# Kernel optimization log

Measured on AMD Instinct MI355X. Metric: run time of the kernel, lower is better.

The kernel has to match this reference:

```python
import jax, jax.numpy as jnp
import numpy as np
import math

B, N = 1, 512
C_S, C_Z, C_H, H = 384, 128, 16, 12
P_Q, P_V, NBINS = 4, 8, 64
OUT_DIM = H * (C_H + P_V * 4 + C_Z)


def setup_inputs() -> dict:
    key = jax.random.key(0)
    ks = jax.random.split(key, 16)
    def rn(k, shape, scale=1.0):
        return jax.random.normal(k, shape, dtype=jnp.float32) * scale
    rotations, _ = jnp.linalg.qr(rn(ks[3], (B, N, 3, 3)))  # orthogonal frames
    w = 0.02
    return {
        "s": rn(ks[0], (B, N, C_S)),
        "z": rn(ks[1], (B, N, N, C_Z)),
        "translations": rn(ks[2], (B, N, 3), 10.0),  # spread over ~0-32 A bins
        "rotations": rotations,
        "Wq": rn(ks[4], (C_S, H * C_H), w), "bq": jnp.zeros((H * C_H,), jnp.float32),
        "Wk": rn(ks[5], (C_S, H * C_H), w), "bk": jnp.zeros((H * C_H,), jnp.float32),
        "Wv": rn(ks[6], (C_S, H * C_H), w), "bv": jnp.zeros((H * C_H,), jnp.float32),
        "Wqp": rn(ks[7], (C_S, H * P_Q * 3), w), "bqp": jnp.zeros((H * P_Q * 3,), jnp.float32),
        "Wkp": rn(ks[8], (C_S, H * P_Q * 3), w), "bkp": jnp.zeros((H * P_Q * 3,), jnp.float32),
        "Wvp": rn(ks[9], (C_S, H * P_V * 3), w), "bvp": jnp.zeros((H * P_V * 3,), jnp.float32),
        "Wb": rn(ks[10], (C_Z, H), w), "bb": jnp.zeros((H,), jnp.float32),
        "emb": rn(ks[11], (NBINS, H), w),
        "scale_logits": jnp.zeros((3, H), jnp.float32),
        "head_weights": jnp.ones((H,), jnp.float32),
        "Wout": rn(ks[12], (OUT_DIM, C_S), w), "bout": jnp.zeros((C_S,), jnp.float32),
    }


def reference(s, z, translations, rotations, Wq, bq, Wk, bk, Wv, bv, Wqp, bqp, Wkp, bkp, Wvp, bvp, Wb, bb, emb, scale_logits, head_weights, Wout, bout):
    b, n, _ = s.shape
    t = translations
    q = (s @ Wq + bq).reshape(b, n, H, C_H)
    k = (s @ Wk + bk).reshape(b, n, H, C_H)
    v = (s @ Wv + bv).reshape(b, n, H, C_H)
    q_pts = (s @ Wqp + bqp).reshape(b, n, H, P_Q, 3)
    k_pts = (s @ Wkp + bkp).reshape(b, n, H, P_Q, 3)
    v_pts = (s @ Wvp + bvp).reshape(b, n, H, P_V, 3)
    # local -> global frame
    q_g = jnp.einsum('bnij,bnhpj->bnhpi', rotations, q_pts) + t[:, :, None, None, :]
    k_g = jnp.einsum('bnij,bnhpj->bnhpi', rotations, k_pts) + t[:, :, None, None, :]
    v_g = jnp.einsum('bnij,bnhpj->bnhpi', rotations, v_pts) + t[:, :, None, None, :]
    scalar_logits = jnp.einsum('bnhc,bmhc->bnmh', q, k) / math.sqrt(C_H)  # [b,n,m,h]
    point_dist = jnp.sum((q_g[:, :, None] - k_g[:, None]) ** 2, axis=-1)  # [b,n,m,h,p]
    point_logits = -0.5 * jnp.sum(point_dist, axis=-1) * head_weights[None, None, None, :]
    pair_bias = z @ Wb + bb  # [b,n,m,h]
    pair_dist = jnp.linalg.norm(t[:, :, None, :] - t[:, None, :, :], axis=-1)  # [b,n,m]
    edges = jnp.linspace(0.0, 32.0, NBINS + 1)
    bins = jnp.clip(jnp.searchsorted(edges, pair_dist, side='left') - 1, 0, NBINS - 1)
    dist_bias = emb[bins]  # [b,n,m,h]
    scales = jnp.stack([
        (pair_dist <= 5.0).astype(s.dtype),
        ((pair_dist > 5.0) & (pair_dist <= 15.0)).astype(s.dtype),
        jnp.ones_like(pair_dist),
    ], axis=-1)  # [b,n,m,3]
    per_head = jax.nn.softmax(scale_logits, axis=0)  # [3,h]
    multiscale = jnp.einsum('bnms,sh->bnmh', scales, per_head)
    logits = scalar_logits + point_logits + pair_bias + dist_bias + multiscale
    attn = jax.nn.softmax(logits.astype(jnp.float32), axis=2).astype(s.dtype)  # over m
    out_scalar = jnp.einsum('bnmh,bmhc->bnhc', attn, v)
    out_pts_g = jnp.einsum('bnmh,bmhpi->bnhpi', attn, v_g)
    # global -> local frame (R^T applied)
    out_pts_l = jnp.einsum('bnji,bnhpj->bnhpi', rotations, out_pts_g - t[:, :, None, None, :])
    out_norms = jnp.linalg.norm(out_pts_l, axis=-1)  # [b,n,h,p]
    pair_feat = jnp.einsum('bnmh,bnmc->bnhc', attn, z)
    feats = jnp.concatenate([
        out_scalar,
        out_pts_l.reshape(b, n, H, P_V * 3),
        out_norms,
        pair_feat,
    ], axis=-1).reshape(b, n, -1)  # [b,n,OUT_DIM]
    return feats @ Wout + bout
```

## Files before the change

### kernel.cpp

```cpp
#include <hip/hip_runtime.h>

#define NTOK 512
#define CS 384
#define CZ 128
#define CH 16
#define HN 12
#define PQ 4
#define PV 8
#define FEAT_DIM 2112
#define HSEG 176

__global__ __launch_bounds__(256) void k_proj(
    const float* __restrict__ s,
    const float* __restrict__ Wq,  const float* __restrict__ bq,
    const float* __restrict__ Wk,  const float* __restrict__ bk,
    const float* __restrict__ Wv,  const float* __restrict__ bv,
    const float* __restrict__ Wqp, const float* __restrict__ bqp,
    const float* __restrict__ Wkp, const float* __restrict__ bkp,
    const float* __restrict__ Wvp, const float* __restrict__ bvp,
    float* __restrict__ qs, float* __restrict__ ksT, float* __restrict__ vs,
    float* __restrict__ raw_g)
{
    __shared__ float s_l[16 * CS];
    __shared__ float Ws[16][64];
    const int t  = threadIdx.x;
    const int n0 = blockIdx.x * 16;

    const float4* sg  = (const float4*)(s + (size_t)n0 * CS);
    float4*       sl4 = (float4*)s_l;
#pragma unroll
    for (int j = 0; j < 6; ++j) sl4[j * 256 + t] = sg[j * 256 + t];

    const int col = blockIdx.y * 64 + (t & 63);
    const int tq  = t >> 6;
    const float* bv_;
    int lc;
    if (col < 192)      { bv_ = bq;  lc = col;       }
    else if (col < 384) { bv_ = bk;  lc = col - 192; }
    else if (col < 576) { bv_ = bv;  lc = col - 384; }
    else if (col < 720) { bv_ = bqp; lc = col - 576; }
    else if (col < 864) { bv_ = bkp; lc = col - 720; }
    else                { bv_ = bvp; lc = col - 864; }

    const int kk_s = t >> 4, cq = t & 15;
    const int gcol = blockIdx.y * 64 + cq * 4;
    const float* Wsrc; int lcs, ncs;
    if (gcol < 192)      { Wsrc = Wq;  lcs = gcol;       ncs = 192; }
    else if (gcol < 384) { Wsrc = Wk;  lcs = gcol - 192; ncs = 192; }
    else if (gcol < 576) { Wsrc = Wv;  lcs = gcol - 384; ncs = 192; }
    else if (gcol < 720) { Wsrc = Wqp; lcs = gcol - 576; ncs = 144; }
    else if (gcol < 864) { Wsrc = Wkp; lcs = gcol - 720; ncs = 144; }
    else                 { Wsrc = Wvp; lcs = gcol - 864; ncs = 288; }

    float a0, a1, a2, a3;
    a0 = a1 = a2 = a3 = bv_[lc];
    __syncthreads();

    for (int ks = 0; ks < CS; ks += 16) {
        float4 w4 = *(const float4*)&Wsrc[(size_t)(ks + kk_s) * ncs + lcs];
        __syncthreads();
        *(float4*)&Ws[kk_s][cq * 4] = w4;
        __syncthreads();
        const float* srow = s_l + tq * 4 * CS + ks;
#pragma unroll
        for (int k4 = 0; k4 < 4; ++k4) {
            float4 s0 = *(const float4*)&srow[k4 * 4];
            float4 s1 = *(const float4*)&srow[CS + k4 * 4];
            float4 s2 = *(const float4*)&srow[2 * CS + k4 * 4];
            float4 s3 = *(const float4*)&srow[3 * CS + k4 * 4];
            float w0 = Ws[k4 * 4 + 0][t & 63];
            float w1 = Ws[k4 * 4 + 1][t & 63];
            float w2 = Ws[k4 * 4 + 2][t & 63];
            float w3 = Ws[k4 * 4 + 3][t & 63];
            a0 += s0.x * w0 + s0.y * w1 + s0.z * w2 + s0.w * w3;
            a1 += s1.x * w0 + s1.y * w1 + s1.z * w2 + s1.w * w3;
            a2 += s2.x * w0 + s2.y * w1 + s2.z * w2 + s2.w * w3;
            a3 += s3.x * w0 + s3.y * w1 + s3.z * w2 + s3.w * w3;
        }
    }

    const int n = n0 + tq * 4;
    if (col < 192) {
        qs[(size_t)(n + 0) * 192 + lc] = a0;
        qs[(size_t)(n + 1) * 192 + lc] = a1;
        qs[(size_t)(n + 2) * 192 + lc] = a2;
        qs[(size_t)(n + 3) * 192 + lc] = a3;
    } else if (col < 384) {
        float* p = ksT + (size_t)lc * NTOK + n;
        p[0] = a0; p[1] = a1; p[2] = a2; p[3] = a3;
    } else if (col < 576) {
        vs[(size_t)(n + 0) * 192 + lc] = a0;
        vs[(size_t)(n + 1) * 192 + lc] = a1;
        vs[(size_t)(n + 2) * 192 + lc] = a2;
        vs[(size_t)(n + 3) * 192 + lc] = a3;
    } else {
        const int pc = col - 576;
        raw_g[(size_t)(n + 0) * 576 + pc] = a0;
        raw_g[(size_t)(n + 1) * 576 + pc] = a1;
        raw_g[(size_t)(n + 2) * 576 + pc] = a2;
        raw_g[(size_t)(n + 3) * 576 + pc] = a3;
    }
}

__global__ __launch_bounds__(256) void k_frame(
    const float* __restrict__ raw_g,
    const float* __restrict__ trans,
    const float* __restrict__ rot,
    float* __restrict__ qg, float* __restrict__ kgT, float* __restrict__ vg,
    float* __restrict__ transT)
{
    const int e = blockIdx.x * 256 + threadIdx.x;
    if (e < 512 * 576) {
        const int n = e / 576, loc = e % 576;
        const int i = loc % 3, base = loc - i;
        const float* rp = raw_g + (size_t)n * 576 + base;
        float x0 = rp[0], x1 = rp[1], x2 = rp[2];
        const float* R = rot + (size_t)n * 9 + i * 3;
        float v = trans[(size_t)n * 3 + i] + R[0] * x0 + R[1] * x1 + R[2] * x2;
        if (loc < 144)      qg[(size_t)n * 144 + loc] = v;
        else if (loc < 288) kgT[(size_t)(loc - 144) * NTOK + n] = v;
        else                vg[(size_t)n * 288 + loc - 288] = v;
    } else {
        const int idx = e - 512 * 576;
        if (idx < 3 * NTOK) {
            const int m = idx / 3, i = idx % 3;
            transT[(size_t)i * NTOK + m] = trans[(size_t)m * 3 + i];
        }
    }
}

__global__ __launch_bounds__(256, 2) void k_mid(
    const float* __restrict__ z,
    const float* __restrict__ qs, const float* __restrict__ ksT,
    const float* __restrict__ qg, const float* __restrict__ kgT,
    const float* __restrict__ trans, const float* __restrict__ transT,
    const float* __restrict__ Wb, const float* __restrict__ bbv,
    const float* __restrict__ emb, const float* __restrict__ slog,
    const float* __restrict__ hw,
    float* __restrict__ attn, float* __restrict__ feats)
{
    __shared__ __align__(16) float lgT[NTOK * HN];
    __shared__ __align__(16) float zl[64 * 132];
    __shared__ __align__(16) float wbT[HN * CZ];
    __shared__ float embl[64 * HN];
    __shared__ float ql[192];
    __shared__ float qgl[144];
    __shared__ float tl[3];
    __shared__ float phl[36];
    __shared__ float hwl[HN];

    const int n = blockIdx.x, t = threadIdx.x;

    for (int i = t; i < CZ * HN; i += 256) {
        const int h = i >> 7, c = i & 127;
        wbT[h * CZ + c] = Wb[(size_t)c * HN + h];
    }
    for (int i = t; i < 64 * HN; i += 256) embl[i] = emb[i];
    if (t < 192) ql[t] = qs[(size_t)n * 192 + t];
    if (t < 144) qgl[t] = qg[(size_t)n * 144 + t];
    if (t < 3)   tl[t] = trans[(size_t)n * 3 + t];
    if (t < HN)  hwl[t] = hw[t];
    if (t >= 64 && t < 64 + HN) {
        const int h = t - 64;
        float s0 = slog[h], s1 = slog[HN + h], s2 = slog[2 * HN + h];
        float mx = fmaxf(s0, fmaxf(s1, s2));
        float e0 = expf(s0 - mx), e1 = expf(s1 - mx), e2 = expf(s2 - mx);
        float inv = 1.f / (e0 + e1 + e2);
        phl[h] = e0 * inv; phl[12 + h] = e1 * inv; phl[24 + h] = e2 * inv;
    }

    const int ml = t & 63, hg = t >> 6, h0 = hg * 3;
    const float bb0 = bbv[h0], bb1 = bbv[h0 + 1], bb2 = bbv[h0 + 2];

    const float* w0 = wbT + (h0 + 0) * CZ;
    const float* w1 = wbT + (h0 + 1) * CZ;
    const float* w2 = wbT + (h0 + 2) * CZ;

    for (int mc = 0; mc < 8; ++mc) {
        __syncthreads();
        {
            const float4* zg = (const float4*)(z + ((size_t)n * NTOK + mc * 64) * CZ);
#pragma unroll
            for (int j = 0; j < 8; ++j) {
                float4 v = zg[j * 256 + t];
                const int f = j * 256 + t;
                const int row = f >> 5, c4 = (f & 31) * 4;
                *(float4*)&zl[row * 132 + c4] = v;
            }
        }
        __syncthreads();

        const int mg = mc * 64 + ml;
        float b0 = bb0, b1 = bb1, b2 = bb2;
        const float* zrow = zl + ml * 132;
#pragma unroll 4
        for (int cq = 0; cq < CZ; cq += 4) {
            float4 zv = *(const float4*)&zrow[cq];
            float4 v0 = *(const float4*)&w0[cq];
            float4 v1 = *(const float4*)&w1[cq];
            float4 v2 = *(const float4*)&w2[cq];
            b0 += zv.x * v0.x + zv.y * v0.y + zv.z * v0.z + zv.w * v0.w;
            b1 += zv.x * v1.x + zv.y * v1.y + zv.z * v1.z + zv.w * v1.w;
            b2 += zv.x * v2.x + zv.y * v2.y + zv.z * v2.z + zv.w * v2.w;
        }
        float dx = tl[0] - transT[mg];
        float dy = tl[1] - transT[NTOK + mg];
        float dz = tl[2] - transT[2 * NTOK + mg];
        float dist = sqrtf(dx * dx + dy * dy + dz * dz);
        int bin = min(63, max(0, (int)ceilf(dist * 2.f) - 1));
        const float in5  = (dist <= 5.f) ? 1.f : 0.f;
        const float in15 = (dist > 5.f && dist <= 15.f) ? 1.f : 0.f;

        float acc[3] = {b0, b1, b2};
#pragma unroll
        for (int k = 0; k < 3; ++k) {
            const int h = h0 + k;
            float sc = 0.f;
            const float* kk = ksT + (size_t)h * CH * NTOK + mg;
            const float* qq = ql + h * CH;
#pragma unroll
            for (int c = 0; c < CH; ++c) sc += qq[c] * kk[(size_t)c * NTOK];
            float sd = 0.f;
            const float* kg = kgT + (size_t)h * 12 * NTOK + mg;
            const float* qp = qgl + h * 12;
#pragma unroll
            for (int i = 0; i < 12; ++i) {
                float d = qp[i] - kg[(size_t)i * NTOK];
                sd += d * d;
            }
            acc[k] += sc * 0.25f - 0.5f * sd * hwl[h]
                    + embl[bin * HN + h]
                    + phl[24 + h] + in5 * phl[h] + in15 * phl[12 + h];
        }
        lgT[mg * HN + h0 + 0] = acc[0];
        lgT[mg * HN + h0 + 1] = acc[1];
        lgT[mg * HN + h0 + 2] = acc[2];
    }
    __syncthreads();

    const int lane = t & 63;
#pragma unroll
    for (int hh = 0; hh < 3; ++hh) {
        const int h = h0 + hh;
        float v[8];
        float mx = -1e30f;
#pragma unroll
        for (int i = 0; i < 8; ++i) {
            v[i] = lgT[(lane + 64 * i) * HN + h];
            mx = fmaxf(mx, v[i]);
        }
#pragma unroll
        for (int off = 32; off; off >>= 1) mx = fmaxf(mx, __shfl_xor(mx, off));
        float sm = 0.f;
#pragma unroll
        for (int i = 0; i < 8; ++i) { v[i] = expf(v[i] - mx); sm += v[i]; }
#pragma unroll
        for (int off = 32; off; off >>= 1) sm += __shfl_xor(sm, off);
        const float inv = 1.f / sm;
        float* arow = attn + ((size_t)n * HN + h) * NTOK;
#pragma unroll
        for (int i = 0; i < 8; ++i) {
            float a = v[i] * inv;
            lgT[(lane + 64 * i) * HN + h] = a;
            arow[lane + 64 * i] = a;
        }
    }
    __syncthreads();

    const int slab = t >> 6;
    const int c2 = (t & 63) * 2;
    float pacc[HN][2];
#pragma unroll
    for (int h = 0; h < HN; ++h) { pacc[h][0] = 0.f; pacc[h][1] = 0.f; }
    const float* zp = z + (size_t)n * NTOK * CZ + (size_t)slab * 128 * CZ + c2;
    const float* lp = lgT + slab * 128 * HN;
#pragma unroll 4
    for (int m = 0; m < 128; ++m) {
        float2 zv = *(const float2*)(zp + (size_t)m * CZ);
        float4 a0 = *(const float4*)&lp[m * HN + 0];
        float4 a1 = *(const float4*)&lp[m * HN + 4];
        float4 a2 = *(const float4*)&lp[m * HN + 8];
        pacc[0][0]  += a0.x * zv.x;  pacc[0][1]  += a0.x * zv.y;
        pacc[1][0]  += a0.y * zv.x;  pacc[1][1]  += a0.y * zv.y;
        pacc[2][0]  += a0.z * zv.x;  pacc[2][1]  += a0.z * zv.y;
        pacc[3][0]  += a0.w * zv.x;  pacc[3][1]  += a0.w * zv.y;
        pacc[4][0]  += a1.x * zv.x;  pacc[4][1]  += a1.x * zv.y;
        pacc[5][0]  += a1.y * zv.x;  pacc[5][1]  += a1.y * zv.y;
        pacc[6][0]  += a1.z * zv.x;  pacc[6][1]  += a1.z * zv.y;
        pacc[7][0]  += a1.w * zv.x;  pacc[7][1]  += a1.w * zv.y;
        pacc[8][0]  += a2.x * zv.x;  pacc[8][1]  += a2.x * zv.y;
        pacc[9][0]  += a2.y * zv.x;  pacc[9][1]  += a2.y * zv.y;
        pacc[10][0] += a2.z * zv.x;  pacc[10][1] += a2.z * zv.y;
        pacc[11][0] += a2.w * zv.x;  pacc[11][1] += a2.w * zv.y;
    }
    float* out_l = zl;
    for (int s = 0; s < 4; ++s) {
        __syncthreads();
        if (slab == s) {
#pragma unroll
            for (int h = 0; h < HN; ++h) {
                float* p = &out_l[h * CZ + c2];
                if (s == 0) { p[0] = pacc[h][0]; p[1] = pacc[h][1]; }
                else        { p[0] += pacc[h][0]; p[1] += pacc[h][1]; }
            }
        }
    }
    __syncthreads();
    for (int i = t; i < HN * CZ; i += 256) {
        const int h = i >> 7, c = i & 127;
        feats[(size_t)n * FEAT_DIM + h * HSEG + 48 + c] = out_l[i];
    }
}

__global__ __launch_bounds__(256) void k_outmm(
    const float* __restrict__ attn,
    const float* __restrict__ vs, const float* __restrict__ vg,
    const float* __restrict__ trans,
    const float* __restrict__ rot,
    float* __restrict__ feats)
{
    __shared__ float As_t[64][33];
    __shared__ float Vs[64][40];
    __shared__ float out_l[32 * 40];
    __shared__ float Rl[32][9];
    __shared__ float tl[32][3];
    const int t   = threadIdx.x;
    const int gn0 = blockIdx.x * 32;
    const int h   = blockIdx.y;

    const int slab  = t >> 6;
    const int w     = t & 63;
    const int n0l   = (w >> 3) * 4;
    const int j0    = (w & 7) * 5;

    float acc[4][5];
#pragma unroll
    for (int i = 0; i < 4; ++i)
#pragma unroll
        for (int k = 0; k < 5; ++k) acc[i][k] = 0.f;

    for (int step = 0; step < 8; ++step) {
        const int mb = step * 64;
        __syncthreads();
#pragma unroll
        for (int jj = 0; jj < 2; ++jj) {
            const int f = t + jj * 256;
            const int n_loc = f >> 4, c4 = f & 15;
            float4 a = *(const float4*)&attn[(((size_t)(gn0 + n_loc)) * HN + h) * NTOK + mb + c4 * 4];
            As_t[c4 * 4 + 0][n_loc] = a.x;
            As_t[c4 * 4 + 1][n_loc] = a.y;
            As_t[c4 * 4 + 2][n_loc] = a.z;
            As_t[c4 * 4 + 3][n_loc] = a.w;
        }
#pragma unroll
        for (int jj = 0; jj < 10; ++jj) {
            const int f = t + jj * 256;
            const int m_loc = f / 40, jv = f % 40;
            float v;
            if (jv < 16) v = vs[(size_t)(mb + m_loc) * 192 + h * 16 + jv];
            else         v = vg[(size_t)(mb + m_loc) * 288 + h * 24 + (jv - 16)];
            Vs[m_loc][jv] = v;
        }
        __syncthreads();
#pragma unroll
        for (int mi = 0; mi < 16; ++mi) {
            const int m = slab * 16 + mi;
            float4 a = *(const float4*)&As_t[m][n0l];
            float vv[5];
#pragma unroll
            for (int k = 0; k < 5; ++k) vv[k] = Vs[m][j0 + k];
            const float av[4] = {a.x, a.y, a.z, a.w};
#pragma unroll
            for (int i = 0; i < 4; ++i)
#pragma unroll
                for (int k = 0; k < 5; ++k)
                    acc[i][k] += av[i] * vv[k];
        }
    }

    for (int s = 0; s < 4; ++s) {
        __syncthreads();
        if (slab == s) {
#pragma unroll
            for (int i = 0; i < 4; ++i)
#pragma unroll
                for (int k = 0; k < 5; ++k) {
                    float* p = &out_l[(n0l + i) * 40 + j0 + k];
                    if (s == 0) *p = acc[i][k];
                    else        *p += acc[i][k];
                }
        }
    }
    for (int i = t; i < 32 * 12; i += 256) {
        const int n_loc = i / 12, r = i % 12;
        if (r < 9) Rl[n_loc][r] = rot[(size_t)(gn0 + n_loc) * 9 + r];
        else       tl[n_loc][r - 9] = trans[(size_t)(gn0 + n_loc) * 3 + (r - 9)];
    }
    __syncthreads();

    for (int f = t; f < 32 * 48; f += 256) {
        const int n_loc = f / 48, j = f % 48;
        const float* sh = &out_l[n_loc * 40];
        float* fp = feats + (size_t)(gn0 + n_loc) * FEAT_DIM + h * HSEG;
        const float* R = Rl[n_loc];
        const float* tv = tl[n_loc];
        if (j < 16) {
            fp[j] = sh[j];
        } else if (j < 40) {
            const int jj = j - 16, p = jj / 3, i = jj % 3;
            float val = 0.f;
#pragma unroll
            for (int q = 0; q < 3; ++q) val += R[q * 3 + i] * (sh[16 + p * 3 + q] - tv[q]);
            fp[16 + jj] = val;
        } else {
            const int p = j - 40;
            float s2 = 0.f;
#pragma unroll
            for (int i = 0; i < 3; ++i) {
                float val = 0.f;
#pragma unroll
                for (int q = 0; q < 3; ++q) val += R[q * 3 + i] * (sh[16 + p * 3 + q] - tv[q]);
                s2 += val * val;
            }
            fp[40 + p] = sqrtf(s2);
        }
    }
}

#define KT 16
__global__ __launch_bounds__(256) void k_outproj(
    const float* __restrict__ feats,
    const float* __restrict__ Wout,
    const float* __restrict__ bout,
    float* __restrict__ out)
{
    __shared__ float As[KT][64];
    __shared__ float Bs[KT][64];
    const int t  = threadIdx.x;
    const int n0 = blockIdx.x * 64;
    const int j0 = blockIdx.y * 64;
    const int k0 = blockIdx.z * HSEG;

    const int arow = t >> 2, akq = (t & 3) * 4;
    const int bkk  = t >> 4, bjq = (t & 15) * 4;
    const int tr   = t >> 4, tc  = t & 15;

    float acc[4][4] = {{0.f}};
    for (int s = 0; s < 11; ++s) {
        const int ks = k0 + s * KT;
        float4 a4 = *(const float4*)&feats[(size_t)(n0 + arow) * FEAT_DIM + ks + akq];
        float4 b4 = *(const float4*)&Wout[(size_t)(ks + bkk) * 384 + j0 + bjq];
        __syncthreads();
        As[akq + 0][arow] = a4.x;
        As[akq + 1][arow] = a4.y;
        As[akq + 2][arow] = a4.z;
        As[akq + 3][arow] = a4.w;
        *(float4*)&Bs[bkk][bjq] = b4;
        __syncthreads();
#pragma unroll
        for (int kk = 0; kk < KT; ++kk) {
            float4 av = *(const float4*)&As[kk][tr * 4];
            float4 bv = *(const float4*)&Bs[kk][tc * 4];
            acc[0][0] += av.x * bv.x; acc[0][1] += av.x * bv.y;
            acc[0][2] += av.x * bv.z; acc[0][3] += av.x * bv.w;
            acc[1][0] += av.y * bv.x; acc[1][1] += av.y * bv.y;
            acc[1][2] += av.y * bv.z; acc[1][3] += av.y * bv.w;
            acc[2][0] += av.z * bv.x; acc[2][1] += av.z * bv.y;
            acc[2][2] += av.z * bv.z; acc[2][3] += av.z * bv.w;
            acc[3][0] += av.w * bv.x; acc[3][1] += av.w * bv.y;
            acc[3][2] += av.w * bv.z; acc[3][3] += av.w * bv.w;
        }
    }

    const bool addb = (blockIdx.z == 0);
#pragma unroll
    for (int i = 0; i < 4; ++i) {
        const int row = n0 + tr * 4 + i;
#pragma unroll
        for (int jj = 0; jj < 4; ++jj) {
            const int col = j0 + tc * 4 + jj;
            float v = acc[i][jj];
            if (addb) v += bout[col];
            atomicAdd(&out[(size_t)row * 384 + col], v);
        }
    }
}

extern "C" void kernel_launch(void* const* d_in, const int* in_sizes, int n_in,
                              void* d_out, int out_size, void* d_ws, size_t ws_size,
                              hipStream_t stream) {
    const float* s     = (const float*)d_in[0];
    const float* z     = (const float*)d_in[1];
    const float* trans = (const float*)d_in[2];
    const float* rot   = (const float*)d_in[3];
    const float* Wq    = (const float*)d_in[4];
    const float* bq    = (const float*)d_in[5];
    const float* Wk    = (const float*)d_in[6];
    const float* bk    = (const float*)d_in[7];
    const float* Wv    = (const float*)d_in[8];
    const float* bv    = (const float*)d_in[9];
    const float* Wqp   = (const float*)d_in[10];
    const float* bqp   = (const float*)d_in[11];
    const float* Wkp   = (const float*)d_in[12];
    const float* bkp   = (const float*)d_in[13];
    const float* Wvp   = (const float*)d_in[14];
    const float* bvp   = (const float*)d_in[15];
    const float* Wb    = (const float*)d_in[16];
    const float* bb    = (const float*)d_in[17];
    const float* emb   = (const float*)d_in[18];
    const float* slog  = (const float*)d_in[19];
    const float* hw    = (const float*)d_in[20];
    const float* Wout  = (const float*)d_in[21];
    const float* bout  = (const float*)d_in[22];

    float* W = (float*)d_ws;
    float* qs     = W;
    float* ksT    = qs + 98304;
    float* vs     = ksT + 98304;
    float* qg     = vs + 98304;
    float* kgT    = qg + 73728;
    float* vg     = kgT + 73728;
    float* transT = vg + 147456;
    float* attn   = transT + 1536;
    float* feats  = attn + 3145728;
    float* raw_g  = feats + 1081344;

    k_proj<<<dim3(32, 18), 256, 0, stream>>>(s, Wq, bq, Wk, bk, Wv, bv,
                                             Wqp, bqp, Wkp, bkp, Wvp, bvp,
                                             qs, ksT, vs, raw_g);
    k_frame<<<1158, 256, 0, stream>>>(raw_g, trans, rot, qg, kgT, vg, transT);
    k_mid<<<512, 256, 0, stream>>>(z, qs, ksT, qg, kgT, trans, transT,
                                   Wb, bb, emb, slog, hw, attn, feats);
    k_outmm<<<dim3(16, 12), 256, 0, stream>>>(attn, vs, vg, trans, rot, feats);
    hipMemsetAsync(d_out, 0, (size_t)NTOK * 384 * sizeof(float), stream);
    k_outproj<<<dim3(8, 6, 12), 256, 0, stream>>>(feats, Wout, bout, (float*)d_out);
}
```

Measured before the change: 384.9 us.

## Split pair-bias projection into a separate wide kernel staged through attn buffer

Moves the z·Wb pair-bias computation out of the per-row k_mid kernel into a new k_bias kernel with 4096 blocks. It writes the bias into the attn buffer, which k_mid then reads and overwrites in place. This removes the large z tile from k_mid's shared memory and raises its occupancy hint from 2 to 4 blocks. In exchange, z is read from global memory one extra time and the bias makes an extra round trip through global memory.

```diff
diff --git a/kernel.cpp b/kernel.cpp
--- a/kernel.cpp
+++ b/kernel.cpp
@@ -129,19 +129,66 @@
     }
 }
 
-__global__ __launch_bounds__(256, 2) void k_mid(
+__global__ __launch_bounds__(256) void k_bias(
+    const float* __restrict__ z,
+    const float* __restrict__ Wb,
+    const float* __restrict__ bbv,
+    float* __restrict__ bias)
+{
+    __shared__ __align__(16) float zl[64 * 132];
+    __shared__ __align__(16) float wbT[HN * CZ];
+    const int t = threadIdx.x;
+    const int n = blockIdx.x >> 3, mc = blockIdx.x & 7;
+
+    for (int i = t; i < CZ * HN; i += 256) {
+        const int h = i >> 7, c = i & 127;
+        wbT[h * CZ + c] = Wb[(size_t)c * HN + h];
+    }
+    {
+        const float4* zg = (const float4*)(z + ((size_t)n * NTOK + mc * 64) * CZ);
+#pragma unroll
+        for (int j = 0; j < 8; ++j) {
+            float4 v = zg[j * 256 + t];
+            const int f = j * 256 + t;
+            const int row = f >> 5, c4 = (f & 31) * 4;
+            *(float4*)&zl[row * 132 + c4] = v;
+        }
+    }
+    __syncthreads();
+
+    const int ml = t & 63, hg = t >> 6, h0 = hg * 3;
+    float b0 = bbv[h0], b1 = bbv[h0 + 1], b2 = bbv[h0 + 2];
+    const float* w0 = wbT + (h0 + 0) * CZ;
+    const float* w1 = wbT + (h0 + 1) * CZ;
+    const float* w2 = wbT + (h0 + 2) * CZ;
+    const float* zrow = zl + ml * 132;
+#pragma unroll 4
+    for (int cq = 0; cq < CZ; cq += 4) {
+        float4 zv = *(const float4*)&zrow[cq];
+        float4 v0 = *(const float4*)&w0[cq];
+        float4 v1 = *(const float4*)&w1[cq];
+        float4 v2 = *(const float4*)&w2[cq];
+        b0 += zv.x * v0.x + zv.y * v0.y + zv.z * v0.z + zv.w * v0.w;
+        b1 += zv.x * v1.x + zv.y * v1.y + zv.z * v1.z + zv.w * v1.w;
+        b2 += zv.x * v2.x + zv.y * v2.y + zv.z * v2.z + zv.w * v2.w;
+    }
+    const int mg = mc * 64 + ml;
+    bias[((size_t)n * HN + h0 + 0) * NTOK + mg] = b0;
+    bias[((size_t)n * HN + h0 + 1) * NTOK + mg] = b1;
+    bias[((size_t)n * HN + h0 + 2) * NTOK + mg] = b2;
+}
+
+__global__ __launch_bounds__(256, 4) void k_mid(
     const float* __restrict__ z,
     const float* __restrict__ qs, const float* __restrict__ ksT,
     const float* __restrict__ qg, const float* __restrict__ kgT,
     const float* __restrict__ trans, const float* __restrict__ transT,
-    const float* __restrict__ Wb, const float* __restrict__ bbv,
     const float* __restrict__ emb, const float* __restrict__ slog,
     const float* __restrict__ hw,
     float* __restrict__ attn, float* __restrict__ feats)
 {
     __shared__ __align__(16) float lgT[NTOK * HN];
-    __shared__ __align__(16) float zl[64 * 132];
-    __shared__ __align__(16) float wbT[HN * CZ];
+    __shared__ __align__(16) float out_l[HN * CZ];
     __shared__ float embl[64 * HN];
     __shared__ float ql[192];
     __shared__ float qgl[144];
@@ -150,11 +197,8 @@
     __shared__ float hwl[HN];
 
     const int n = blockIdx.x, t = threadIdx.x;
-
-    for (int i = t; i < CZ * HN; i += 256) {
-        const int h = i >> 7, c = i & 127;
-        wbT[h * CZ + c] = Wb[(size_t)c * HN + h];
-    }
+    const int ml = t & 63, hg = t >> 6, h0 = hg * 3;
+
     for (int i = t; i < 64 * HN; i += 256) embl[i] = emb[i];
     if (t < 192) ql[t] = qs[(size_t)n * 192 + t];
     if (t < 144) qgl[t] = qg[(size_t)n * 144 + t];
@@ -168,41 +212,15 @@
         float inv = 1.f / (e0 + e1 + e2);
         phl[h] = e0 * inv; phl[12 + h] = e1 * inv; phl[24 + h] = e2 * inv;
     }
-
-    const int ml = t & 63, hg = t >> 6, h0 = hg * 3;
-    const float bb0 = bbv[h0], bb1 = bbv[h0 + 1], bb2 = bbv[h0 + 2];
-
-    const float* w0 = wbT + (h0 + 0) * CZ;
-    const float* w1 = wbT + (h0 + 1) * CZ;
-    const float* w2 = wbT + (h0 + 2) * CZ;
+    __syncthreads();
+
+    const float* brow = attn + ((size_t)n * HN + h0) * NTOK;
 
     for (int mc = 0; mc < 8; ++mc) {
-        __syncthreads();
-        {
-            const float4* zg = (const float4*)(z + ((size_t)n * NTOK + mc * 64) * CZ);
-#pragma unroll
-            for (int j = 0; j < 8; ++j) {
-                float4 v = zg[j * 256 + t];
-                const int f = j * 256 + t;
-                const int row = f >> 5, c4 = (f & 31) * 4;
-                *(float4*)&zl[row * 132 + c4] = v;
-            }
-        }
-        __syncthreads();
-
         const int mg = mc * 64 + ml;
-        float b0 = bb0, b1 = bb1, b2 = bb2;
-        const float* zrow = zl + ml * 132;
-#pragma unroll 4
-        for (int cq = 0; cq < CZ; cq += 4) {
-            float4 zv = *(const float4*)&zrow[cq];
-            float4 v0 = *(const float4*)&w0[cq];
-            float4 v1 = *(const float4*)&w1[cq];
-            float4 v2 = *(const float4*)&w2[cq];
-            b0 += zv.x * v0.x + zv.y * v0.y + zv.z * v0.z + zv.w * v0.w;
-            b1 += zv.x * v1.x + zv.y * v1.y + zv.z * v1.z + zv.w * v1.w;
-            b2 += zv.x * v2.x + zv.y * v2.y + zv.z * v2.z + zv.w * v2.w;
-        }
+        float b0 = brow[mg];
+        float b1 = brow[NTOK + mg];
+        float b2 = brow[2 * NTOK + mg];
         float dx = tl[0] - transT[mg];
         float dy = tl[1] - transT[NTOK + mg];
         float dz = tl[2] - transT[2 * NTOK + mg];
@@ -236,7 +254,6 @@
         lgT[mg * HN + h0 + 1] = acc[1];
         lgT[mg * HN + h0 + 2] = acc[2];
     }
-    __syncthreads();
 
     const int lane = t & 63;
 #pragma unroll
@@ -267,8 +284,8 @@
     }
     __syncthreads();
 
-    const int slab = t >> 6;
-    const int c2 = (t & 63) * 2;
+    const int slab = hg;
+    const int c2 = ml * 2;
     float pacc[HN][2];
 #pragma unroll
     for (int h = 0; h < HN; ++h) { pacc[h][0] = 0.f; pacc[h][1] = 0.f; }
@@ -293,7 +310,6 @@
         pacc[10][0] += a2.z * zv.x;  pacc[10][1] += a2.z * zv.y;
         pacc[11][0] += a2.w * zv.x;  pacc[11][1] += a2.w * zv.y;
     }
-    float* out_l = zl;
     for (int s = 0; s < 4; ++s) {
         __syncthreads();
         if (slab == s) {
@@ -525,12 +541,13 @@
     float* feats  = attn + 3145728;
     float* raw_g  = feats + 1081344;
 
+    k_bias<<<4096, 256, 0, stream>>>(z, Wb, bb, attn);
     k_proj<<<dim3(32, 18), 256, 0, stream>>>(s, Wq, bq, Wk, bk, Wv, bv,
                                              Wqp, bqp, Wkp, bkp, Wvp, bvp,
                                              qs, ksT, vs, raw_g);
     k_frame<<<1158, 256, 0, stream>>>(raw_g, trans, rot, qg, kgT, vg, transT);
     k_mid<<<512, 256, 0, stream>>>(z, qs, ksT, qg, kgT, trans, transT,
-                                   Wb, bb, emb, slog, hw, attn, feats);
+                                   emb, slog, hw, attn, feats);
     k_outmm<<<dim3(16, 12), 256, 0, stream>>>(attn, vs, vg, trans, rot, feats);
     hipMemsetAsync(d_out, 0, (size_t)NTOK * 384 * sizeof(float), stream);
     k_outproj<<<dim3(8, 6, 12), 256, 0, stream>>>(feats, Wout, bout, (float*)d_out);
```

Result: slower. 494.9 us (+28.6%).
